# Performance work log

Hardware: AMD Instinct MI355X
Metric: run time of the kernel (lower is better)

## Reference

```python
import jax, jax.numpy as jnp
import numpy as np


def setup_inputs() -> dict:
    key = jax.random.key(0)
    k1, k2, k3, k4 = jax.random.split(key, 4)
    N, D, H = 16384, 128, 256
    features = jax.random.normal(k1, (N, D), dtype=jnp.float32)
    adj_matrix = jax.random.randint(k2, (N, N), 0, 2, dtype=jnp.int32)
    # Linear(2D -> H) and Linear(D -> H), torch convention W: [out, in]
    Wd = jax.random.normal(k3, (H, 2 * D), dtype=jnp.float32) * (1.0 / np.sqrt(2 * D))
    bd = jnp.zeros((H,), dtype=jnp.float32)
    Wo = jax.random.normal(k4, (H, D), dtype=jnp.float32) * (1.0 / np.sqrt(D))
    bo = jnp.zeros((H,), dtype=jnp.float32)
    return {"features": features, "adj_matrix": adj_matrix,
            "Wd": Wd, "bd": bd, "Wo": Wo, "bo": bo}


def reference(features, adj_matrix, Wd, bd, Wo, bo):
    # Faithful math, but without materializing the O(N^2*2D) pairwise tensor:
    #   sum_j adj[i,j] * concat(f[i], f[j]) = concat(deg[i]*f[i], (adj @ f)[i])
    adj = adj_matrix.astype(features.dtype)
    deg = jnp.sum(adj, axis=-1, keepdims=True)              # [N,1]
    neigh_mask = jnp.max(adj, axis=-1, keepdims=True)       # [N,1]
    neigh_num = deg + (1.0 - neigh_mask)                    # avoid div by 0
    head_sum = features * deg                                # [N,D]
    tail_sum = adj @ features                                # [N,D]
    neigh_ave = jnp.concatenate([head_sum, tail_sum], axis=-1) / neigh_num  # [N,2D]
    neigh_feat = neigh_ave @ Wd.T + bd                       # [N,H]
    updated = (features @ Wo.T + bo) - neigh_feat            # [N,H]
    updated = jnp.tanh(updated)
    # dropout is identity in eval mode; withAgg=False returns the pair
    return (updated, updated)
```

## Files before the change

kernel.cpp:

```cpp
#include <hip/hip_runtime.h>
#include <hip/hip_bf16.h>

#define NROW 16384
#define DIM 128
#define HOUT 256
#define SPLIT 4

typedef float f32x4 __attribute__((ext_vector_type(4)));
typedef __bf16 bf16x8 __attribute__((ext_vector_type(8)));
typedef unsigned int u32;
typedef unsigned int u32x4 __attribute__((ext_vector_type(4)));

__global__ void k_transpose(const float* __restrict__ f, short* __restrict__ fT,
                            float* __restrict__ deg) {
    __shared__ short tr[128][72];
    const int t = threadIdx.x;
    const int j0 = blockIdx.x * 64;
    if (blockIdx.x < 64) deg[blockIdx.x * 256 + t] = 0.f;
    for (int it = 0; it < 8; ++it) {
        int slot = t + 256 * it;
        int j = slot >> 5;
        int dq = slot & 31;
        f32x4 v = *reinterpret_cast<const f32x4*>(f + (size_t)(j0 + j) * DIM + dq * 4);
#pragma unroll
        for (int c = 0; c < 4; ++c) {
            __hip_bfloat16 h = __float2bfloat16(v[c]);
            tr[dq * 4 + c][j] = *reinterpret_cast<short*>(&h);
        }
    }
    __syncthreads();
    for (int it = 0; it < 4; ++it) {
        int slot = t + 256 * it;
        int d = slot >> 3;
        int c8 = slot & 7;
        int4 v = *reinterpret_cast<const int4*>(&tr[d][c8 * 8]);
        *reinterpret_cast<int4*>(fT + (size_t)d * NROW + j0 + c8 * 8) = v;
    }
}

__device__ inline bf16x8 cvt_a(const int4& a, const int4& b, int& ds) {
    union { u32x4 u; bf16x8 f; } U;
    U.u.x = (a.x ? 0x3F80u : 0u) | (a.y ? 0x3F800000u : 0u);
    U.u.y = (a.z ? 0x3F80u : 0u) | (a.w ? 0x3F800000u : 0u);
    U.u.z = (b.x ? 0x3F80u : 0u) | (b.y ? 0x3F800000u : 0u);
    U.u.w = (b.z ? 0x3F80u : 0u) | (b.w ? 0x3F800000u : 0u);
    ds += a.x + a.y + a.z + a.w + b.x + b.y + b.z + b.w;
    return U.f;
}

__global__ __launch_bounds__(256, 2) void k_gemm(const int* __restrict__ adj,
                                                 const short* __restrict__ fT,
                                                 float* __restrict__ part,
                                                 float* __restrict__ deg) {
    const int t = threadIdx.x;
    const int rb = blockIdx.x >> 2;
    const int s  = blockIdx.x & 3;
    const int i0 = rb * 128;
    const int kb0 = s * (NROW / SPLIT);
    const int lane = t & 63;
    const int w = t >> 6;
    const int lr = lane & 15;
    const int lk = (lane >> 4) * 8;

    f32x4 acc[2][8] = {};
    int dsum[2] = {0, 0};

    const int* aptr0 = adj + (size_t)(i0 + w * 32 + lr) * NROW + kb0 + lk;
    const int* aptr1 = aptr0 + (size_t)16 * NROW;
    const short* bptr = fT + (size_t)lr * NROW + kb0 + lk;

    for (int it = 0; it < (NROW / SPLIT) / 32; ++it) {
        const int ko = it * 32;
        int4 a0a = *reinterpret_cast<const int4*>(aptr0 + ko);
        int4 a0b = *reinterpret_cast<const int4*>(aptr0 + ko + 4);
        int4 a1a = *reinterpret_cast<const int4*>(aptr1 + ko);
        int4 a1b = *reinterpret_cast<const int4*>(aptr1 + ko + 4);
        bf16x8 bf[8];
#pragma unroll
        for (int ci = 0; ci < 8; ++ci)
            bf[ci] = *reinterpret_cast<const bf16x8*>(bptr + (size_t)ci * 16 * NROW + ko);
        bf16x8 af0 = cvt_a(a0a, a0b, dsum[0]);
        bf16x8 af1 = cvt_a(a1a, a1b, dsum[1]);
#pragma unroll
        for (int ci = 0; ci < 8; ++ci) {
            acc[0][ci] = __builtin_amdgcn_mfma_f32_16x16x32_bf16(af0, bf[ci], acc[0][ci], 0, 0, 0);
            acc[1][ci] = __builtin_amdgcn_mfma_f32_16x16x32_bf16(af1, bf[ci], acc[1][ci], 0, 0, 0);
        }
    }
#pragma unroll
    for (int ti = 0; ti < 2; ++ti)
#pragma unroll
        for (int ci = 0; ci < 8; ++ci)
#pragma unroll
            for (int r = 0; r < 4; ++r) {
                int i = i0 + w * 32 + ti * 16 + (lane >> 4) * 4 + r;
                int d = ci * 16 + lr;
                part[((size_t)s * NROW + i) * DIM + d] = acc[ti][ci][r];
            }
#pragma unroll
    for (int ti = 0; ti < 2; ++ti) {
        float v = (float)dsum[ti];
        v += __shfl_xor(v, 16);
        v += __shfl_xor(v, 32);
        if (lane < 16) atomicAdd(deg + i0 + w * 32 + ti * 16 + lr, v);
    }
}

__global__ __launch_bounds__(256, 2) void k_epilogue(const float* __restrict__ feat,
                                                     const float* __restrict__ part,
                                                     const float* __restrict__ deg,
                                                     const float* __restrict__ Wd,
                                                     const float* __restrict__ bd,
                                                     const float* __restrict__ Wo,
                                                     const float* __restrict__ bo,
                                                     float* __restrict__ out) {
    __shared__ float fs[32][132];
    __shared__ float tn[32][132];
    __shared__ float mrow[32], inv[32];
    const int t = threadIdx.x;
    const int i0 = blockIdx.x * 32;
    if (t < 32) {
        float d = deg[i0 + t];
        mrow[t] = d > 0.f ? 1.f : 0.f;
        inv[t]  = d > 0.f ? 1.f / d : 1.f;
    }
    __syncthreads();
    for (int it = 0; it < 4; ++it) {
        int slot = t + 256 * it;
        int r = slot >> 5, dq = slot & 31;
        size_t gi = (size_t)(i0 + r) * DIM + dq * 4;
        f32x4 fv = *reinterpret_cast<const f32x4*>(feat + gi);
        *reinterpret_cast<f32x4*>(&fs[r][dq * 4]) = fv;
        f32x4 p = *reinterpret_cast<const f32x4*>(part + gi);
#pragma unroll
        for (int sp = 1; sp < SPLIT; ++sp)
            p += *reinterpret_cast<const f32x4*>(part + (size_t)sp * NROW * DIM + gi);
        f32x4 tv = p * inv[r];
        *reinterpret_cast<f32x4*>(&tn[r][dq * 4]) = tv;
    }
    __syncthreads();
    const int rt = t & 7;
    const int ht = t >> 3;
    float accM[4][8] = {};
    float accB[4][8] = {};
    for (int d = 0; d < DIM; d += 4) {
        f32x4 fr[4], tr[4];
#pragma unroll
        for (int rr = 0; rr < 4; ++rr) {
            fr[rr] = *reinterpret_cast<const f32x4*>(&fs[rt * 4 + rr][d]);
            tr[rr] = *reinterpret_cast<const f32x4*>(&tn[rt * 4 + rr][d]);
        }
#pragma unroll
        for (int hh = 0; hh < 8; ++hh) {
            int h = ht * 8 + hh;
            f32x4 wo = *reinterpret_cast<const f32x4*>(Wo + (size_t)h * DIM + d);
            f32x4 w1 = *reinterpret_cast<const f32x4*>(Wd + (size_t)h * 2 * DIM + d);
            f32x4 w2 = *reinterpret_cast<const f32x4*>(Wd + (size_t)h * 2 * DIM + DIM + d);
#pragma unroll
            for (int rr = 0; rr < 4; ++rr)
#pragma unroll
                for (int c = 0; c < 4; ++c) {
                    accM[rr][hh] += fr[rr][c] * wo[c] - tr[rr][c] * w2[c];
                    accB[rr][hh] += fr[rr][c] * w1[c];
                }
        }
    }
    f32x4 bo0 = *reinterpret_cast<const f32x4*>(bo + ht * 8);
    f32x4 bo1 = *reinterpret_cast<const f32x4*>(bo + ht * 8 + 4);
    f32x4 bd0 = *reinterpret_cast<const f32x4*>(bd + ht * 8);
    f32x4 bd1 = *reinterpret_cast<const f32x4*>(bd + ht * 8 + 4);
#pragma unroll
    for (int rr = 0; rr < 4; ++rr) {
        int i = i0 + rt * 4 + rr;
        float m = mrow[rt * 4 + rr];
        f32x4 v0, v1;
#pragma unroll
        for (int c = 0; c < 4; ++c) {
            v0[c] = tanhf(accM[rr][c]     - m * accB[rr][c]     + bo0[c] - bd0[c]);
            v1[c] = tanhf(accM[rr][c + 4] - m * accB[rr][c + 4] + bo1[c] - bd1[c]);
        }
        float* o = out + (size_t)i * HOUT + ht * 8;
        *reinterpret_cast<f32x4*>(o) = v0;
        *reinterpret_cast<f32x4*>(o + 4) = v1;
        float* o2 = o + (size_t)NROW * HOUT;
        *reinterpret_cast<f32x4*>(o2) = v0;
        *reinterpret_cast<f32x4*>(o2 + 4) = v1;
    }
}

extern "C" void kernel_launch(void* const* d_in, const int* in_sizes, int n_in,
                              void* d_out, int out_size, void* d_ws, size_t ws_size,
                              hipStream_t stream) {
    const float* feat = (const float*)d_in[0];
    const int*   adj  = (const int*)d_in[1];
    const float* Wd   = (const float*)d_in[2];
    const float* bd   = (const float*)d_in[3];
    const float* Wo   = (const float*)d_in[4];
    const float* bo   = (const float*)d_in[5];
    float* out = (float*)d_out;
    char* ws = (char*)d_ws;
    short* fT   = (short*)ws;
    float* part = (float*)(ws + (size_t)4  * 1024 * 1024);
    float* deg  = (float*)(ws + (size_t)40 * 1024 * 1024);
    k_transpose<<<256, 256, 0, stream>>>(feat, fT, deg);
    k_gemm     <<<512, 256, 0, stream>>>(adj, fT, part, deg);
    k_epilogue <<<512, 256, 0, stream>>>(feat, part, deg, Wd, bd, Wo, bo, out);
}
```

Before: 1.602 ms.

## Halve GEMM block rows, split columns across waves, double-buffer register loads

Each GEMM block now covers 64 rows instead of 128, and its four waves form a 2x2 grid so each wave computes 32 rows by 64 feature columns. The grid doubles to 1024 blocks and launch bounds allow four blocks per CU. A two-stage register double buffer prefetches the next k-tile while MFMAs run on the current one. The cost is that every adjacency tile is now loaded by two waves, so adjacency traffic doubles, and the final prefetch wraps around to issue one wasted load.

```diff
diff --git a/kernel.cpp b/kernel.cpp
--- a/kernel.cpp
+++ b/kernel.cpp
@@ -48,61 +48,79 @@
     return U.f;
 }
 
-__global__ __launch_bounds__(256, 2) void k_gemm(const int* __restrict__ adj,
+struct Regs { int4 a0a, a0b, a1a, a1b; bf16x8 b[4]; };
+
+__device__ inline void load_tile(Regs& R, const int* aptr0, const int* aptr1,
+                                 const short* bptr, int ko) {
+    R.a0a = *reinterpret_cast<const int4*>(aptr0 + ko);
+    R.a0b = *reinterpret_cast<const int4*>(aptr0 + ko + 4);
+    R.a1a = *reinterpret_cast<const int4*>(aptr1 + ko);
+    R.a1b = *reinterpret_cast<const int4*>(aptr1 + ko + 4);
+#pragma unroll
+    for (int ci = 0; ci < 4; ++ci)
+        R.b[ci] = *reinterpret_cast<const bf16x8*>(bptr + (size_t)ci * 16 * NROW + ko);
+}
+
+__device__ inline void compute_tile(Regs& R, f32x4 (&acc)[2][4], int (&dsum)[2]) {
+    bf16x8 af0 = cvt_a(R.a0a, R.a0b, dsum[0]);
+    bf16x8 af1 = cvt_a(R.a1a, R.a1b, dsum[1]);
+#pragma unroll
+    for (int ci = 0; ci < 4; ++ci) {
+        acc[0][ci] = __builtin_amdgcn_mfma_f32_16x16x32_bf16(af0, R.b[ci], acc[0][ci], 0, 0, 0);
+        acc[1][ci] = __builtin_amdgcn_mfma_f32_16x16x32_bf16(af1, R.b[ci], acc[1][ci], 0, 0, 0);
+    }
+}
+
+__global__ __launch_bounds__(256, 4) void k_gemm(const int* __restrict__ adj,
                                                  const short* __restrict__ fT,
                                                  float* __restrict__ part,
                                                  float* __restrict__ deg) {
     const int t = threadIdx.x;
     const int rb = blockIdx.x >> 2;
     const int s  = blockIdx.x & 3;
-    const int i0 = rb * 128;
+    const int i0 = rb * 64;
     const int kb0 = s * (NROW / SPLIT);
     const int lane = t & 63;
     const int w = t >> 6;
+    const int wr = w >> 1;
+    const int wc = w & 1;
     const int lr = lane & 15;
     const int lk = (lane >> 4) * 8;
 
-    f32x4 acc[2][8] = {};
+    f32x4 acc[2][4] = {};
     int dsum[2] = {0, 0};
 
-    const int* aptr0 = adj + (size_t)(i0 + w * 32 + lr) * NROW + kb0 + lk;
+    const int* aptr0 = adj + (size_t)(i0 + wr * 32 + lr) * NROW + kb0 + lk;
     const int* aptr1 = aptr0 + (size_t)16 * NROW;
-    const short* bptr = fT + (size_t)lr * NROW + kb0 + lk;
-
-    for (int it = 0; it < (NROW / SPLIT) / 32; ++it) {
-        const int ko = it * 32;
-        int4 a0a = *reinterpret_cast<const int4*>(aptr0 + ko);
-        int4 a0b = *reinterpret_cast<const int4*>(aptr0 + ko + 4);
-        int4 a1a = *reinterpret_cast<const int4*>(aptr1 + ko);
-        int4 a1b = *reinterpret_cast<const int4*>(aptr1 + ko + 4);
-        bf16x8 bf[8];
-#pragma unroll
-        for (int ci = 0; ci < 8; ++ci)
-            bf[ci] = *reinterpret_cast<const bf16x8*>(bptr + (size_t)ci * 16 * NROW + ko);
-        bf16x8 af0 = cvt_a(a0a, a0b, dsum[0]);
-        bf16x8 af1 = cvt_a(a1a, a1b, dsum[1]);
-#pragma unroll
-        for (int ci = 0; ci < 8; ++ci) {
-            acc[0][ci] = __builtin_amdgcn_mfma_f32_16x16x32_bf16(af0, bf[ci], acc[0][ci], 0, 0, 0);
-            acc[1][ci] = __builtin_amdgcn_mfma_f32_16x16x32_bf16(af1, bf[ci], acc[1][ci], 0, 0, 0);
-        }
+    const short* bptr = fT + (size_t)(wc * 64 + lr) * NROW + kb0 + lk;
+
+    Regs R0, R1;
+    load_tile(R0, aptr0, aptr1, bptr, 0);
+#pragma unroll 1
+    for (int it = 0; it < 128; it += 2) {
+        load_tile(R1, aptr0, aptr1, bptr, (it + 1) * 32);
+        compute_tile(R0, acc, dsum);
+        load_tile(R0, aptr0, aptr1, bptr, ((it + 2) & 127) * 32);
+        compute_tile(R1, acc, dsum);
     }
 #pragma unroll
     for (int ti = 0; ti < 2; ++ti)
 #pragma unroll
-        for (int ci = 0; ci < 8; ++ci)
+        for (int ci = 0; ci < 4; ++ci)
 #pragma unroll
             for (int r = 0; r < 4; ++r) {
-                int i = i0 + w * 32 + ti * 16 + (lane >> 4) * 4 + r;
-                int d = ci * 16 + lr;
+                int i = i0 + wr * 32 + ti * 16 + (lane >> 4) * 4 + r;
+                int d = wc * 64 + ci * 16 + lr;
                 part[((size_t)s * NROW + i) * DIM + d] = acc[ti][ci][r];
             }
-#pragma unroll
-    for (int ti = 0; ti < 2; ++ti) {
-        float v = (float)dsum[ti];
-        v += __shfl_xor(v, 16);
-        v += __shfl_xor(v, 32);
-        if (lane < 16) atomicAdd(deg + i0 + w * 32 + ti * 16 + lr, v);
+    if (wc == 0) {
+#pragma unroll
+        for (int ti = 0; ti < 2; ++ti) {
+            float v = (float)dsum[ti];
+            v += __shfl_xor(v, 16);
+            v += __shfl_xor(v, 32);
+            if (lane < 16) atomicAdd(deg + i0 + wr * 32 + ti * 16 + lr, v);
+        }
     }
 }
 
@@ -202,7 +220,7 @@
     short* fT   = (short*)ws;
     float* part = (float*)(ws + (size_t)4  * 1024 * 1024);
     float* deg  = (float*)(ws + (size_t)40 * 1024 * 1024);
-    k_transpose<<<256, 256, 0, stream>>>(feat, fT, deg);
-    k_gemm     <<<512, 256, 0, stream>>>(adj, fT, part, deg);
-    k_epilogue <<<512, 256, 0, stream>>>(feat, part, deg, Wd, bd, Wo, bo, out);
-}
+    k_transpose<<<256,  256, 0, stream>>>(feat, fT, deg);
+    k_gemm     <<<1024, 256, 0, stream>>>(adj, fT, part, deg);
+    k_epilogue <<<512,  256, 0, stream>>>(feat, part, deg, Wd, bd, Wo, bo, out);
+}
```

After: 1.855 ms. +15.8%, slower.

## Double-buffer gemm global loads with inline asm and explicit waitcnt

Applied to the files above, without the earlier changes.

Rewrites the adjacency×features GEMM main loop to issue global loads via inline-asm global_load_dwordx4 with SGPR bases and a shared 32-bit VGPR offset. Two register tile sets are kept in flight, so loads for the next pair of k-steps are issued right after computing the current pair. This aims to hide memory latency and cut address-computation VGPR/VALU work. In exchange it raises register pressure, and the waitcnt vmcnt(0) before each compute pair can still stall on outstanding loads.

```diff
diff --git a/kernel.cpp b/kernel.cpp
--- a/kernel.cpp
+++ b/kernel.cpp
@@ -8,6 +8,7 @@
 
 typedef float f32x4 __attribute__((ext_vector_type(4)));
 typedef __bf16 bf16x8 __attribute__((ext_vector_type(8)));
+typedef int v4i __attribute__((ext_vector_type(4)));
 typedef unsigned int u32;
 typedef unsigned int u32x4 __attribute__((ext_vector_type(4)));
 
@@ -38,15 +39,21 @@
     }
 }
 
-__device__ inline bf16x8 cvt_a(const int4& a, const int4& b, int& ds) {
+__device__ inline bf16x8 cvt8(v4i a, v4i b, int& ds) {
     union { u32x4 u; bf16x8 f; } U;
-    U.u.x = (a.x ? 0x3F80u : 0u) | (a.y ? 0x3F800000u : 0u);
-    U.u.y = (a.z ? 0x3F80u : 0u) | (a.w ? 0x3F800000u : 0u);
-    U.u.z = (b.x ? 0x3F80u : 0u) | (b.y ? 0x3F800000u : 0u);
-    U.u.w = (b.z ? 0x3F80u : 0u) | (b.w ? 0x3F800000u : 0u);
-    ds += a.x + a.y + a.z + a.w + b.x + b.y + b.z + b.w;
+    U.u[0] = (a[0] ? 0x3F80u : 0u) | (a[1] ? 0x3F800000u : 0u);
+    U.u[1] = (a[2] ? 0x3F80u : 0u) | (a[3] ? 0x3F800000u : 0u);
+    U.u[2] = (b[0] ? 0x3F80u : 0u) | (b[1] ? 0x3F800000u : 0u);
+    U.u[3] = (b[2] ? 0x3F80u : 0u) | (b[3] ? 0x3F800000u : 0u);
+    ds += a[0] + a[1] + a[2] + a[3] + b[0] + b[1] + b[2] + b[3];
     return U.f;
 }
+__device__ inline bf16x8 as_bf(v4i v) { union { v4i i; bf16x8 f; } U; U.i = v; return U.f; }
+
+#define GLD(dst, voff, base) \
+    asm volatile("global_load_dwordx4 %0, %1, %2" : "=v"(dst) : "v"(voff), "s"(base))
+#define GLD16(dst, voff, base) \
+    asm volatile("global_load_dwordx4 %0, %1, %2 offset:16" : "=v"(dst) : "v"(voff), "s"(base))
 
 __global__ __launch_bounds__(256, 2) void k_gemm(const int* __restrict__ adj,
                                                  const short* __restrict__ fT,
@@ -63,30 +70,67 @@
     const int lk = (lane >> 4) * 8;
 
     f32x4 acc[2][8] = {};
-    int dsum[2] = {0, 0};
-
-    const int* aptr0 = adj + (size_t)(i0 + w * 32 + lr) * NROW + kb0 + lk;
-    const int* aptr1 = aptr0 + (size_t)16 * NROW;
-    const short* bptr = fT + (size_t)lr * NROW + kb0 + lk;
-
-    for (int it = 0; it < (NROW / SPLIT) / 32; ++it) {
-        const int ko = it * 32;
-        int4 a0a = *reinterpret_cast<const int4*>(aptr0 + ko);
-        int4 a0b = *reinterpret_cast<const int4*>(aptr0 + ko + 4);
-        int4 a1a = *reinterpret_cast<const int4*>(aptr1 + ko);
-        int4 a1b = *reinterpret_cast<const int4*>(aptr1 + ko + 4);
-        bf16x8 bf[8];
-#pragma unroll
-        for (int ci = 0; ci < 8; ++ci)
-            bf[ci] = *reinterpret_cast<const bf16x8*>(bptr + (size_t)ci * 16 * NROW + ko);
-        bf16x8 af0 = cvt_a(a0a, a0b, dsum[0]);
-        bf16x8 af1 = cvt_a(a1a, a1b, dsum[1]);
-#pragma unroll
-        for (int ci = 0; ci < 8; ++ci) {
-            acc[0][ci] = __builtin_amdgcn_mfma_f32_16x16x32_bf16(af0, bf[ci], acc[0][ci], 0, 0, 0);
-            acc[1][ci] = __builtin_amdgcn_mfma_f32_16x16x32_bf16(af1, bf[ci], acc[1][ci], 0, 0, 0);
-        }
-    }
+    int dsum0 = 0, dsum1 = 0;
+
+    const int*   adjLo = adj;
+    const int*   adjHi = adj + (size_t)16 * NROW;
+    const short* fT0 = fT;
+    const short* fT1 = fT + (size_t)16 * NROW;
+    const short* fT2 = fT + (size_t)32 * NROW;
+    const short* fT3 = fT + (size_t)48 * NROW;
+    const short* fT4 = fT + (size_t)64 * NROW;
+    const short* fT5 = fT + (size_t)80 * NROW;
+    const short* fT6 = fT + (size_t)96 * NROW;
+    const short* fT7 = fT + (size_t)112 * NROW;
+    u32 ofsA = (u32)((i0 + w * 32 + lr) * NROW + kb0 + lk) * 4u;
+    u32 ofsB = (u32)(lr * NROW + kb0 + lk) * 2u;
+
+    v4i T0Aa, T0Ab, T0Ac, T0Ad, T0B0, T0B1, T0B2, T0B3, T0B4, T0B5, T0B6, T0B7;
+    v4i T1Aa, T1Ab, T1Ac, T1Ad, T1B0, T1B1, T1B2, T1B3, T1B4, T1B5, T1B6, T1B7;
+
+#define ISSUE(P)                                                        \
+    do {                                                                \
+        GLD  (P##Aa, ofsA, adjLo);  GLD16(P##Ab, ofsA, adjLo);          \
+        GLD  (P##Ac, ofsA, adjHi);  GLD16(P##Ad, ofsA, adjHi);          \
+        GLD(P##B0, ofsB, fT0);  GLD(P##B1, ofsB, fT1);                  \
+        GLD(P##B2, ofsB, fT2);  GLD(P##B3, ofsB, fT3);                  \
+        GLD(P##B4, ofsB, fT4);  GLD(P##B5, ofsB, fT5);                  \
+        GLD(P##B6, ofsB, fT6);  GLD(P##B7, ofsB, fT7);                  \
+        ofsA += 128u;  ofsB += 64u;                                     \
+    } while (0)
+
+#define WAIT0                                         \
+    do {                                              \
+        asm volatile("s_waitcnt vmcnt(0)");           \
+        __builtin_amdgcn_sched_barrier(0);            \
+    } while (0)
+
+#define MM(P, ci)                                                                            \
+    acc[0][ci] = __builtin_amdgcn_mfma_f32_16x16x32_bf16(af0, as_bf(P##B##ci), acc[0][ci], 0, 0, 0); \
+    acc[1][ci] = __builtin_amdgcn_mfma_f32_16x16x32_bf16(af1, as_bf(P##B##ci), acc[1][ci], 0, 0, 0)
+
+#define COMPUTE(P)                                    \
+    do {                                              \
+        bf16x8 af0 = cvt8(P##Aa, P##Ab, dsum0);       \
+        bf16x8 af1 = cvt8(P##Ac, P##Ad, dsum1);       \
+        MM(P, 0); MM(P, 1); MM(P, 2); MM(P, 3);       \
+        MM(P, 4); MM(P, 5); MM(P, 6); MM(P, 7);       \
+    } while (0)
+
+    ISSUE(T0);
+    ISSUE(T1);
+#pragma unroll 1
+    for (int it = 0; it < 126; it += 2) {
+        WAIT0;
+        COMPUTE(T0);
+        COMPUTE(T1);
+        ISSUE(T0);
+        ISSUE(T1);
+    }
+    WAIT0;
+    COMPUTE(T0);
+    COMPUTE(T1);
+
 #pragma unroll
     for (int ti = 0; ti < 2; ++ti)
 #pragma unroll
@@ -97,13 +141,22 @@
                 int d = ci * 16 + lr;
                 part[((size_t)s * NROW + i) * DIM + d] = acc[ti][ci][r];
             }
-#pragma unroll
-    for (int ti = 0; ti < 2; ++ti) {
-        float v = (float)dsum[ti];
-        v += __shfl_xor(v, 16);
-        v += __shfl_xor(v, 32);
-        if (lane < 16) atomicAdd(deg + i0 + w * 32 + ti * 16 + lr, v);
-    }
+    {
+        float v0 = (float)dsum0;
+        v0 += __shfl_xor(v0, 16);
+        v0 += __shfl_xor(v0, 32);
+        float v1 = (float)dsum1;
+        v1 += __shfl_xor(v1, 16);
+        v1 += __shfl_xor(v1, 32);
+        if (lane < 16) {
+            atomicAdd(deg + i0 + w * 32 + lr, v0);
+            atomicAdd(deg + i0 + w * 32 + 16 + lr, v1);
+        }
+    }
+#undef ISSUE
+#undef WAIT0
+#undef MM
+#undef COMPUTE
 }
 
 __global__ __launch_bounds__(256, 2) void k_epilogue(const float* __restrict__ feat,
```

After: 1.604 ms. Within noise of the previous version (+0.1%).

## Stage GEMM tiles through LDS with async global_load_lds double buffering

Applied to the files above, without the earlier changes.

The adjacency GEMM now copies A (int adjacency) and B (bf16 transposed features) tiles into double-buffered shared memory using global_load_lds, prefetching the next k-tile while MFMAs run on the current one. Operands are then read from LDS instead of being loaded straight from global memory in registers. This aims to hide global memory latency on the bandwidth-bound 1 GiB adjacency stream and to cut redundant B loads across waves. In exchange it adds a block-wide barrier every step and uses more shared memory, and the unpadded LDS reads may hit bank conflicts.

```diff
diff --git a/kernel.cpp b/kernel.cpp
--- a/kernel.cpp
+++ b/kernel.cpp
@@ -8,6 +8,7 @@
 
 typedef float f32x4 __attribute__((ext_vector_type(4)));
 typedef __bf16 bf16x8 __attribute__((ext_vector_type(8)));
+typedef int v4i __attribute__((ext_vector_type(4)));
 typedef unsigned int u32;
 typedef unsigned int u32x4 __attribute__((ext_vector_type(4)));
 
@@ -38,20 +39,27 @@
     }
 }
 
-__device__ inline bf16x8 cvt_a(const int4& a, const int4& b, int& ds) {
+__device__ inline bf16x8 cvt8(v4i a, v4i b, int& ds) {
     union { u32x4 u; bf16x8 f; } U;
-    U.u.x = (a.x ? 0x3F80u : 0u) | (a.y ? 0x3F800000u : 0u);
-    U.u.y = (a.z ? 0x3F80u : 0u) | (a.w ? 0x3F800000u : 0u);
-    U.u.z = (b.x ? 0x3F80u : 0u) | (b.y ? 0x3F800000u : 0u);
-    U.u.w = (b.z ? 0x3F80u : 0u) | (b.w ? 0x3F800000u : 0u);
-    ds += a.x + a.y + a.z + a.w + b.x + b.y + b.z + b.w;
+    U.u[0] = (a[0] ? 0x3F80u : 0u) | (a[1] ? 0x3F800000u : 0u);
+    U.u[1] = (a[2] ? 0x3F80u : 0u) | (a[3] ? 0x3F800000u : 0u);
+    U.u[2] = (b[0] ? 0x3F80u : 0u) | (b[1] ? 0x3F800000u : 0u);
+    U.u[3] = (b[2] ? 0x3F80u : 0u) | (b[3] ? 0x3F800000u : 0u);
+    ds += a[0] + a[1] + a[2] + a[3] + b[0] + b[1] + b[2] + b[3];
     return U.f;
 }
+
+#define GLOAD16(g, l)                                                         \
+    __builtin_amdgcn_global_load_lds(                                         \
+        (const __attribute__((address_space(1))) unsigned int*)(g),           \
+        (__attribute__((address_space(3))) unsigned int*)(l), 16, 0, 0)
 
 __global__ __launch_bounds__(256, 2) void k_gemm(const int* __restrict__ adj,
                                                  const short* __restrict__ fT,
                                                  float* __restrict__ part,
                                                  float* __restrict__ deg) {
+    __shared__ int   As[2][128][32];
+    __shared__ short Fs[2][128][32];
     const int t = threadIdx.x;
     const int rb = blockIdx.x >> 2;
     const int s  = blockIdx.x & 3;
@@ -60,33 +68,55 @@
     const int lane = t & 63;
     const int w = t >> 6;
     const int lr = lane & 15;
-    const int lk = (lane >> 4) * 8;
+    const int lk8 = lane >> 4;
 
     f32x4 acc[2][8] = {};
-    int dsum[2] = {0, 0};
-
-    const int* aptr0 = adj + (size_t)(i0 + w * 32 + lr) * NROW + kb0 + lk;
-    const int* aptr1 = aptr0 + (size_t)16 * NROW;
-    const short* bptr = fT + (size_t)lr * NROW + kb0 + lk;
-
-    for (int it = 0; it < (NROW / SPLIT) / 32; ++it) {
-        const int ko = it * 32;
-        int4 a0a = *reinterpret_cast<const int4*>(aptr0 + ko);
-        int4 a0b = *reinterpret_cast<const int4*>(aptr0 + ko + 4);
-        int4 a1a = *reinterpret_cast<const int4*>(aptr1 + ko);
-        int4 a1b = *reinterpret_cast<const int4*>(aptr1 + ko + 4);
-        bf16x8 bf[8];
+    int dsum0 = 0, dsum1 = 0;
+
+#define STAGE(cur, kb)                                                            \
+    do {                                                                          \
+        _Pragma("unroll")                                                         \
+        for (int r = 0; r < 4; ++r) {                                             \
+            int uslot = r * 256 + w * 64;                                         \
+            int slot = uslot + lane;                                              \
+            const int* g = adj + (size_t)(i0 + (slot >> 3)) * NROW + (kb) + (slot & 7) * 4; \
+            GLOAD16(g, (char*)&As[cur][0][0] + (size_t)uslot * 16);               \
+        }                                                                         \
+        _Pragma("unroll")                                                         \
+        for (int r = 0; r < 2; ++r) {                                             \
+            int uslot = r * 256 + w * 64;                                         \
+            int slot = uslot + lane;                                              \
+            const short* g = fT + (size_t)(slot >> 2) * NROW + (kb) + (slot & 3) * 8; \
+            GLOAD16(g, (char*)&Fs[cur][0][0] + (size_t)uslot * 16);               \
+        }                                                                         \
+    } while (0)
+
+    STAGE(0, kb0);
+    __syncthreads();
+
+    int cur = 0;
+#pragma unroll 1
+    for (int step = 0; step < 128; ++step) {
+        if (step + 1 < 128) STAGE(cur ^ 1, kb0 + (step + 1) * 32);
+        bf16x8 bfr[8];
 #pragma unroll
         for (int ci = 0; ci < 8; ++ci)
-            bf[ci] = *reinterpret_cast<const bf16x8*>(bptr + (size_t)ci * 16 * NROW + ko);
-        bf16x8 af0 = cvt_a(a0a, a0b, dsum[0]);
-        bf16x8 af1 = cvt_a(a1a, a1b, dsum[1]);
+            bfr[ci] = *reinterpret_cast<const bf16x8*>(&Fs[cur][ci * 16 + lr][lk8 * 8]);
+        v4i a0 = *reinterpret_cast<const v4i*>(&As[cur][w * 32 + lr][lk8 * 8]);
+        v4i a1 = *reinterpret_cast<const v4i*>(&As[cur][w * 32 + lr][lk8 * 8 + 4]);
+        v4i a2 = *reinterpret_cast<const v4i*>(&As[cur][w * 32 + 16 + lr][lk8 * 8]);
+        v4i a3 = *reinterpret_cast<const v4i*>(&As[cur][w * 32 + 16 + lr][lk8 * 8 + 4]);
+        bf16x8 af0 = cvt8(a0, a1, dsum0);
+        bf16x8 af1 = cvt8(a2, a3, dsum1);
 #pragma unroll
         for (int ci = 0; ci < 8; ++ci) {
-            acc[0][ci] = __builtin_amdgcn_mfma_f32_16x16x32_bf16(af0, bf[ci], acc[0][ci], 0, 0, 0);
-            acc[1][ci] = __builtin_amdgcn_mfma_f32_16x16x32_bf16(af1, bf[ci], acc[1][ci], 0, 0, 0);
-        }
-    }
+            acc[0][ci] = __builtin_amdgcn_mfma_f32_16x16x32_bf16(af0, bfr[ci], acc[0][ci], 0, 0, 0);
+            acc[1][ci] = __builtin_amdgcn_mfma_f32_16x16x32_bf16(af1, bfr[ci], acc[1][ci], 0, 0, 0);
+        }
+        __syncthreads();
+        cur ^= 1;
+    }
+
 #pragma unroll
     for (int ti = 0; ti < 2; ++ti)
 #pragma unroll
@@ -97,13 +127,19 @@
                 int d = ci * 16 + lr;
                 part[((size_t)s * NROW + i) * DIM + d] = acc[ti][ci][r];
             }
-#pragma unroll
-    for (int ti = 0; ti < 2; ++ti) {
-        float v = (float)dsum[ti];
-        v += __shfl_xor(v, 16);
-        v += __shfl_xor(v, 32);
-        if (lane < 16) atomicAdd(deg + i0 + w * 32 + ti * 16 + lr, v);
-    }
+    {
+        float v0 = (float)dsum0;
+        v0 += __shfl_xor(v0, 16);
+        v0 += __shfl_xor(v0, 32);
+        float v1 = (float)dsum1;
+        v1 += __shfl_xor(v1, 16);
+        v1 += __shfl_xor(v1, 32);
+        if (lane < 16) {
+            atomicAdd(deg + i0 + w * 32 + lr, v0);
+            atomicAdd(deg + i0 + w * 32 + 16 + lr, v1);
+        }
+    }
+#undef STAGE
 }
 
 __global__ __launch_bounds__(256, 2) void k_epilogue(const float* __restrict__ feat,
```

Measured after the change: 1.431 ms. 1.12x faster.
